# Optimization experiments

Measured on AMD Instinct MI355X. Metric: run time of the kernel, lower is better.

## Reference

```python
import jax, jax.numpy as jnp
import numpy as np

T, H, I, E, TOPK = 1024, 1024, 2816, 16, 4


def setup_inputs() -> dict:
    key = jax.random.key(0)
    ks = jax.random.split(key, 5)
    s_h = 1.0 / np.sqrt(H)
    s_i = 1.0 / np.sqrt(I)
    return {
        "x": jax.random.normal(ks[0], (T, H), jnp.float32),
        "Wg": jax.random.normal(ks[1], (E, H), jnp.float32) * s_h,
        "gate_w": jax.random.normal(ks[2], (E, H, I), jnp.float32) * s_h,
        "up_w": jax.random.normal(ks[3], (E, H, I), jnp.float32) * s_h,
        "down_w": jax.random.normal(ks[4], (E, I, H), jnp.float32) * s_i,
        "top_k": TOPK,
    }


def reference(x, Wg, gate_w, up_w, down_w, top_k):
    # Router: softmax over expert logits, top-k, renormalize
    logits = x @ Wg.T                                   # [T, E]
    probs = jax.nn.softmax(logits, axis=-1)
    topk_w, topk_ids = jax.lax.top_k(probs, top_k)      # [T, K]
    topk_w = topk_w / jnp.sum(topk_w, axis=-1, keepdims=True)

    # Dense combine weights [T, E]: zero for unselected experts -> exact same
    # math as the per-token dispatch loop in the original module.
    n_tok = x.shape[0]
    combine = jnp.zeros((n_tok, Wg.shape[0]), x.dtype)
    combine = combine.at[jnp.arange(n_tok)[:, None], topk_ids].add(topk_w)

    # SwiGLU per expert, batched over the expert axis
    g = jax.nn.silu(jnp.einsum('th,ehi->eti', x, gate_w))  # [E, T, I]
    u = jnp.einsum('th,ehi->eti', x, up_w)                 # [E, T, I]
    y = jnp.einsum('eti,eih->eth', g * u, down_w)          # [E, T, H]

    # Weighted combine across experts
    return jnp.einsum('eth,te->th', y, combine)            # [T, H]
```

## Files before the change

kernel.cpp:

```cpp
#include <hip/hip_runtime.h>

static constexpr int cT = 1024;
static constexpr int cH = 1024;
static constexpr int cI = 2816;
static constexpr int cE = 16;
static constexpr int cK = 4;

typedef __attribute__((ext_vector_type(8))) short bf16x8;
typedef __attribute__((ext_vector_type(4))) float f32x4;
typedef __attribute__((ext_vector_type(4))) unsigned uint4v;
typedef __attribute__((ext_vector_type(2))) unsigned uint2v;

__device__ __forceinline__ unsigned f2bf(float f) {
  unsigned u = __float_as_uint(f);
  return (u + 0x7FFFu + ((u >> 16) & 1u)) >> 16;
}
__device__ __forceinline__ unsigned pack2(float lo, float hi) {
  return f2bf(lo) | (f2bf(hi) << 16);
}

__global__ __launch_bounds__(256) void xcast_kernel(
    const float* __restrict__ x, unsigned short* __restrict__ xb) {
  const int i = blockIdx.x * 256 + threadIdx.x;
  const float4* xv = (const float4*)x;
  const float4 a = xv[i * 2], b = xv[i * 2 + 1];
  uint4v o;
  o.x = pack2(a.x, a.y); o.y = pack2(a.z, a.w);
  o.z = pack2(b.x, b.y); o.w = pack2(b.z, b.w);
  ((uint4v*)xb)[i] = o;
}

__global__ __launch_bounds__(64) void router_kernel(
    const float* __restrict__ x, const float* __restrict__ Wg,
    int* __restrict__ topk_id, float* __restrict__ topk_w,
    int* __restrict__ counts) {
  const int t = blockIdx.x;
  const int l = threadIdx.x;

  float xa[16];
#pragma unroll
  for (int i = 0; i < 16; ++i) xa[i] = x[(size_t)t * cH + l + 64 * i];

  float lg[16];
#pragma unroll
  for (int e = 0; e < 16; ++e) {
    float s = 0.f;
#pragma unroll
    for (int i = 0; i < 16; ++i) s += xa[i] * Wg[(size_t)e * cH + l + 64 * i];
#pragma unroll
    for (int d = 1; d < 64; d <<= 1) s += __shfl_xor(s, d);
    lg[e] = s;
  }

  if (l == 0) {
    int ids[4]; float vals[4];
    unsigned taken = 0;
#pragma unroll
    for (int j = 0; j < 4; ++j) {
      float m = -1e30f; int mi = 0;
#pragma unroll
      for (int e = 0; e < 16; ++e) {
        bool better = !((taken >> e) & 1u) && lg[e] > m;
        if (better) { m = lg[e]; mi = e; }
      }
      taken |= 1u << mi; ids[j] = mi; vals[j] = m;
    }
    const float mx = vals[0];
    float s = 0.f;
#pragma unroll
    for (int j = 0; j < 4; ++j) { vals[j] = __expf(vals[j] - mx); s += vals[j]; }
    const float inv = 1.f / s;
#pragma unroll
    for (int j = 0; j < 4; ++j) {
      topk_id[t * 4 + j] = ids[j];
      topk_w[t * 4 + j] = vals[j] * inv;
      atomicAdd(&counts[ids[j]], 1);
    }
  }
}

__global__ void scan_kernel(const int* __restrict__ counts,
                            int* __restrict__ offsets) {
  if (threadIdx.x == 0 && blockIdx.x == 0) {
    int acc = 0;
    for (int e = 0; e < cE; ++e) { offsets[e] = acc; acc += counts[e]; }
    offsets[cE] = acc;
  }
}

__global__ __launch_bounds__(256) void scatter_kernel(
    const int* __restrict__ topk_id, const float* __restrict__ topk_w,
    const int* __restrict__ offsets, int* __restrict__ cursor,
    int* __restrict__ pair_token, float* __restrict__ pair_w) {
  const int i = blockIdx.x * 256 + threadIdx.x;
  const int t = i >> 2;
  const int e = topk_id[i];
  const int pos = offsets[e] + atomicAdd(&cursor[e], 1);
  pair_token[pos] = t;
  pair_w[pos] = topk_w[i];
}

__global__ __launch_bounds__(256, 2) void gateup_kernel(
    const unsigned short* __restrict__ xb, const float* __restrict__ gw,
    const float* __restrict__ uw, const int* __restrict__ offsets,
    const int* __restrict__ pair_token, unsigned short* __restrict__ act) {
  const int e = blockIdx.y;
  const int off = offsets[e];
  const int n_e = offsets[e + 1] - off;
  if (n_e <= 0) return;
  const int nb = blockIdx.x * 64;
  const int tid = threadIdx.x;
  const int l = tid & 63, w = tid >> 6;
  const int wm = w * 64;

  __shared__ unsigned sB[2 * 2048];
  __shared__ int tokl[256];

  const int mat = tid >> 7;
  const int bg_ = (tid >> 4) & 7;
  const int bq  = tid & 15;
  const float* wp = (mat ? uw : gw) + (size_t)e * cH * cI + nb;

  for (int m0 = 0; m0 < n_e; m0 += 256) {
    const int rows = min(256, n_e - m0);
    tokl[tid] = pair_token[off + m0 + min(tid, rows - 1)];
    __syncthreads();

    const unsigned short* ap[4];
#pragma unroll
    for (int mi = 0; mi < 4; ++mi) {
      const int r = min(wm + mi * 16 + (l & 15), rows - 1);
      ap[mi] = xb + (size_t)tokl[r] * cH + (l >> 4) * 8;
    }

    f32x4 ag[4][4], au[4][4];
#pragma unroll
    for (int mi = 0; mi < 4; ++mi)
#pragma unroll
      for (int ni = 0; ni < 4; ++ni) {
        ag[mi][ni].x = 0.f; ag[mi][ni].y = 0.f; ag[mi][ni].z = 0.f; ag[mi][ni].w = 0.f;
        au[mi][ni].x = 0.f; au[mi][ni].y = 0.f; au[mi][ni].z = 0.f; au[mi][ni].w = 0.f;
      }

    for (int kt = 0; kt < cH / 64; ++kt) {
      bf16x8 av[4][2];
#pragma unroll
      for (int mi = 0; mi < 4; ++mi)
#pragma unroll
        for (int ks = 0; ks < 2; ++ks)
          av[mi][ks] = *(const bf16x8*)(ap[mi] + kt * 64 + ks * 32);

#pragma unroll
      for (int j = 0; j < 4; ++j) {
        const int c = bq + 16 * j;
        const float* p = wp + (size_t)(kt * 64 + bg_ * 8) * cI + c;
        const float f0 = p[0];
        const float f1 = p[(size_t)cI];
        const float f2 = p[(size_t)2 * cI];
        const float f3 = p[(size_t)3 * cI];
        const float f4 = p[(size_t)4 * cI];
        const float f5 = p[(size_t)5 * cI];
        const float f6 = p[(size_t)6 * cI];
        const float f7 = p[(size_t)7 * cI];
        uint4v P;
        P.x = pack2(f0, f1); P.y = pack2(f2, f3);
        P.z = pack2(f4, f5); P.w = pack2(f6, f7);
        *(uint4v*)&sB[mat * 2048 + (bg_ * 64 + c) * 4] = P;
      }
      __syncthreads();

#pragma unroll
      for (int ks = 0; ks < 2; ++ks) {
        const int gidx = ks * 4 + (l >> 4);
#pragma unroll
        for (int ni = 0; ni < 4; ++ni) {
          const int bi = (gidx * 64 + ni * 16 + (l & 15)) * 4;
          const bf16x8 bgf = *(const bf16x8*)&sB[bi];
          const bf16x8 buf_ = *(const bf16x8*)&sB[2048 + bi];
#pragma unroll
          for (int mi = 0; mi < 4; ++mi) {
            ag[mi][ni] = __builtin_amdgcn_mfma_f32_16x16x32_bf16(av[mi][ks], bgf, ag[mi][ni], 0, 0, 0);
            au[mi][ni] = __builtin_amdgcn_mfma_f32_16x16x32_bf16(av[mi][ks], buf_, au[mi][ni], 0, 0, 0);
          }
        }
      }
      __syncthreads();
    }

#pragma unroll
    for (int mi = 0; mi < 4; ++mi)
#pragma unroll
      for (int j = 0; j < 4; ++j) {
        const int er = m0 + wm + mi * 16 + (l >> 4) * 4 + j;
        if (er < n_e) {
#pragma unroll
          for (int ni = 0; ni < 4; ++ni) {
            const float g = ag[mi][ni][j], u = au[mi][ni][j];
            const float v = (g / (1.f + __expf(-g))) * u;
            act[(size_t)(off + er) * cI + nb + ni * 16 + (l & 15)] =
                (unsigned short)f2bf(v);
          }
        }
      }
  }
}

__global__ __launch_bounds__(256, 2) void down_kernel(
    const unsigned short* __restrict__ act, const float* __restrict__ dw,
    const int* __restrict__ offsets, const int* __restrict__ pair_token,
    const float* __restrict__ pair_w, float* __restrict__ out) {
  const int e = blockIdx.y;
  const int off = offsets[e];
  const int n_e = offsets[e + 1] - off;
  if (n_e <= 0) return;
  const int nb = blockIdx.x * 64;
  const int tid = threadIdx.x;
  const int l = tid & 63, w = tid >> 6;
  const int wm = w * 80;

  __shared__ unsigned sB[2048];

  const int bg_ = tid >> 5;
  const int bq  = (tid >> 1) & 15;
  const int bh  = tid & 1;
  const float* wp = dw + (size_t)e * cI * cH + nb;

  for (int m0 = 0; m0 < n_e; m0 += 320) {
    const unsigned short* ap[5];
#pragma unroll
    for (int mi = 0; mi < 5; ++mi) {
      const int r = min(m0 + wm + mi * 16 + (l & 15), n_e - 1);
      ap[mi] = act + (size_t)(off + r) * cI + (l >> 4) * 8;
    }

    f32x4 acc[5][4];
#pragma unroll
    for (int mi = 0; mi < 5; ++mi)
#pragma unroll
      for (int ni = 0; ni < 4; ++ni) {
        acc[mi][ni].x = 0.f; acc[mi][ni].y = 0.f;
        acc[mi][ni].z = 0.f; acc[mi][ni].w = 0.f;
      }

    for (int kt = 0; kt < cI / 64; ++kt) {
      bf16x8 av[5][2];
#pragma unroll
      for (int mi = 0; mi < 5; ++mi)
#pragma unroll
        for (int ks = 0; ks < 2; ++ks)
          av[mi][ks] = *(const bf16x8*)(ap[mi] + kt * 64 + ks * 32);

#pragma unroll
      for (int j = 0; j < 4; ++j) {
        const int c = bq + 16 * j;
        const float* p = wp + (size_t)(kt * 64 + bg_ * 8 + bh * 4) * cH + c;
        const float f0 = p[0];
        const float f1 = p[(size_t)cH];
        const float f2 = p[(size_t)2 * cH];
        const float f3 = p[(size_t)3 * cH];
        uint2v P;
        P.x = pack2(f0, f1); P.y = pack2(f2, f3);
        *(uint2v*)((char*)sB + (bg_ * 64 + c) * 16 + bh * 8) = P;
      }
      __syncthreads();

#pragma unroll
      for (int ks = 0; ks < 2; ++ks) {
        const int gidx = ks * 4 + (l >> 4);
#pragma unroll
        for (int ni = 0; ni < 4; ++ni) {
          const bf16x8 b = *(const bf16x8*)&sB[(gidx * 64 + ni * 16 + (l & 15)) * 4];
#pragma unroll
          for (int mi = 0; mi < 5; ++mi)
            acc[mi][ni] = __builtin_amdgcn_mfma_f32_16x16x32_bf16(av[mi][ks], b, acc[mi][ni], 0, 0, 0);
        }
      }
      __syncthreads();
    }

#pragma unroll
    for (int mi = 0; mi < 5; ++mi)
#pragma unroll
      for (int j = 0; j < 4; ++j) {
        const int er = m0 + wm + mi * 16 + (l >> 4) * 4 + j;
        if (er < n_e) {
          const int pr = off + er;
          const int t = pair_token[pr];
          const float wgt = pair_w[pr];
#pragma unroll
          for (int ni = 0; ni < 4; ++ni)
            atomicAdd(out + (size_t)t * cH + nb + ni * 16 + (l & 15),
                      wgt * acc[mi][ni][j]);
        }
      }
  }
}

extern "C" void kernel_launch(void* const* d_in, const int* in_sizes, int n_in,
                              void* d_out, int out_size, void* d_ws,
                              size_t ws_size, hipStream_t stream) {
  (void)in_sizes; (void)n_in; (void)out_size; (void)ws_size;
  const float* x = (const float*)d_in[0];
  const float* Wg = (const float*)d_in[1];
  const float* gw = (const float*)d_in[2];
  const float* uw = (const float*)d_in[3];
  const float* dw = (const float*)d_in[4];
  float* out = (float*)d_out;

  char* ws = (char*)d_ws;
  int* counts     = (int*)(ws + 0);
  int* cursor     = (int*)(ws + 64);
  int* offsets    = (int*)(ws + 128);
  int* topk_id    = (int*)(ws + 256);
  float* topk_w   = (float*)(ws + 256 + 16384);
  int* pair_token = (int*)(ws + 256 + 32768);
  float* pair_w   = (float*)(ws + 256 + 49152);
  unsigned short* act = (unsigned short*)(ws + 65792);
  unsigned short* xb  = (unsigned short*)(ws + 65792 + (size_t)4096 * 2816 * 2);

  hipMemsetAsync(ws, 0, 128, stream);
  hipMemsetAsync(d_out, 0, (size_t)cT * cH * sizeof(float), stream);

  xcast_kernel<<<cT * cH / (256 * 8), 256, 0, stream>>>(x, xb);
  router_kernel<<<cT, 64, 0, stream>>>(x, Wg, topk_id, topk_w, counts);
  scan_kernel<<<1, 1, 0, stream>>>(counts, offsets);
  scatter_kernel<<<cT * cK / 256, 256, 0, stream>>>(topk_id, topk_w, offsets,
                                                    cursor, pair_token, pair_w);
  gateup_kernel<<<dim3(cI / 64, cE), 256, 0, stream>>>(xb, gw, uw, offsets,
                                                       pair_token, act);
  down_kernel<<<dim3(cH / 64, cE), 256, 0, stream>>>(act, dw, offsets,
                                                     pair_token, pair_w, out);
}
```

Baseline: 454.2 us.

## Split MoE GEMMs over token chunks, prefetch weights, replace atomics with combine

Gate/up and down kernels now split each expert's tokens into 128-row chunks spread across three blocks per column strip, which raises parallelism and occupancy. Weight tiles are loaded with float4 reads, prefetched into registers one k-step ahead and written to a padded, double-buffered LDS layout, so one barrier per k-step replaces two. The down kernel writes unweighted per-pair outputs to a workspace, and a new combine kernel sums the four expert rows per token. This removes the atomic adds and the memset of the output, at the cost of an extra fp32 buffer and one more kernel launch. Each expert's weights are now streamed by several blocks instead of one, which adds redundant weight traffic.

```diff
diff --git a/kernel.cpp b/kernel.cpp
--- a/kernel.cpp
+++ b/kernel.cpp
@@ -8,8 +8,8 @@
 
 typedef __attribute__((ext_vector_type(8))) short bf16x8;
 typedef __attribute__((ext_vector_type(4))) float f32x4;
+typedef __attribute__((ext_vector_type(2))) unsigned uint2v;
 typedef __attribute__((ext_vector_type(4))) unsigned uint4v;
-typedef __attribute__((ext_vector_type(2))) unsigned uint2v;
 
 __device__ __forceinline__ unsigned f2bf(float f) {
   unsigned u = __float_as_uint(f);
@@ -17,6 +17,13 @@
 }
 __device__ __forceinline__ unsigned pack2(float lo, float hi) {
   return f2bf(lo) | (f2bf(hi) << 16);
+}
+
+__device__ __forceinline__ bf16x8 ld_bfrag(const unsigned* p) {
+  union { uint2v d[2]; bf16x8 v; } r;
+  r.d[0] = *(const uint2v*)p;
+  r.d[1] = *(const uint2v*)(p + 2);
+  return r.v;
 }
 
 __global__ __launch_bounds__(256) void xcast_kernel(
@@ -89,109 +96,113 @@
 }
 
 __global__ __launch_bounds__(256) void scatter_kernel(
-    const int* __restrict__ topk_id, const float* __restrict__ topk_w,
-    const int* __restrict__ offsets, int* __restrict__ cursor,
-    int* __restrict__ pair_token, float* __restrict__ pair_w) {
+    const int* __restrict__ topk_id, const int* __restrict__ offsets,
+    int* __restrict__ cursor, int* __restrict__ pair_token,
+    int* __restrict__ pair_pos) {
   const int i = blockIdx.x * 256 + threadIdx.x;
   const int t = i >> 2;
   const int e = topk_id[i];
   const int pos = offsets[e] + atomicAdd(&cursor[e], 1);
   pair_token[pos] = t;
-  pair_w[pos] = topk_w[i];
-}
-
-__global__ __launch_bounds__(256, 2) void gateup_kernel(
+  pair_pos[i] = pos;
+}
+
+__global__ __launch_bounds__(256, 3) void gateup_kernel(
     const unsigned short* __restrict__ xb, const float* __restrict__ gw,
     const float* __restrict__ uw, const int* __restrict__ offsets,
     const int* __restrict__ pair_token, unsigned short* __restrict__ act) {
   const int e = blockIdx.y;
   const int off = offsets[e];
   const int n_e = offsets[e + 1] - off;
-  if (n_e <= 0) return;
-  const int nb = blockIdx.x * 64;
-  const int tid = threadIdx.x;
-  const int l = tid & 63, w = tid >> 6;
-  const int wm = w * 64;
-
-  __shared__ unsigned sB[2 * 2048];
-  __shared__ int tokl[256];
-
-  const int mat = tid >> 7;
-  const int bg_ = (tid >> 4) & 7;
-  const int bq  = tid & 15;
-  const float* wp = (mat ? uw : gw) + (size_t)e * cH * cI + nb;
-
-  for (int m0 = 0; m0 < n_e; m0 += 256) {
-    const int rows = min(256, n_e - m0);
-    tokl[tid] = pair_token[off + m0 + min(tid, rows - 1)];
+  const int strip = blockIdx.x / 3;
+  const int c0 = (blockIdx.x % 3) * 128;
+  if (c0 >= n_e) return;
+  const int nb = strip * 64;
+  const int tid = threadIdx.x, l = tid & 63, w = tid >> 6;
+
+  __shared__ unsigned sB[2][2][2176];
+  __shared__ int tokl[128];
+
+  const int sa = tid >> 4;
+  const int sc = tid & 15;
+  const float* gb = gw + (size_t)e * cH * cI + nb + sc * 4;
+  const float* ub = uw + (size_t)e * cH * cI + nb + sc * 4;
+
+  for (int m0 = c0; m0 < n_e; m0 += 384) {
+    if (tid < 128) tokl[tid] = pair_token[off + min(m0 + tid, n_e - 1)];
     __syncthreads();
-
-    const unsigned short* ap[4];
-#pragma unroll
-    for (int mi = 0; mi < 4; ++mi) {
-      const int r = min(wm + mi * 16 + (l & 15), rows - 1);
-      ap[mi] = xb + (size_t)tokl[r] * cH + (l >> 4) * 8;
-    }
-
-    f32x4 ag[4][4], au[4][4];
-#pragma unroll
-    for (int mi = 0; mi < 4; ++mi)
+    const int rows = min(128, n_e - m0);
+
+    const unsigned short* ap[2];
+#pragma unroll
+    for (int mi = 0; mi < 2; ++mi) {
+      const int idx = min(w * 32 + mi * 16 + (l & 15), rows - 1);
+      ap[mi] = xb + (size_t)tokl[idx] * cH + (l >> 4) * 8;
+    }
+
+    f32x4 ag[2][4], au[2][4];
+#pragma unroll
+    for (int mi = 0; mi < 2; ++mi)
 #pragma unroll
       for (int ni = 0; ni < 4; ++ni) {
-        ag[mi][ni].x = 0.f; ag[mi][ni].y = 0.f; ag[mi][ni].z = 0.f; ag[mi][ni].w = 0.f;
-        au[mi][ni].x = 0.f; au[mi][ni].y = 0.f; au[mi][ni].z = 0.f; au[mi][ni].w = 0.f;
-      }
-
-    for (int kt = 0; kt < cH / 64; ++kt) {
-      bf16x8 av[4][2];
-#pragma unroll
-      for (int mi = 0; mi < 4; ++mi)
+        ag[mi][ni] = (f32x4){0.f, 0.f, 0.f, 0.f};
+        au[mi][ni] = (f32x4){0.f, 0.f, 0.f, 0.f};
+      }
+
+    float4 rg[4], ru[4];
+#pragma unroll
+    for (int j = 0; j < 4; ++j) {
+      rg[j] = *(const float4*)(gb + (size_t)(sa * 4 + j) * cI);
+      ru[j] = *(const float4*)(ub + (size_t)(sa * 4 + j) * cI);
+    }
+
+    for (int kt = 0; kt < 16; ++kt) {
+      const int cur = kt & 1;
+      const int wbase = (sc * 4) * 34 + sa * 2;
+#pragma unroll
+      for (int i = 0; i < 4; ++i) {
+        uint2v pg, pu;
+        pg.x = pack2(rg[0][i], rg[1][i]); pg.y = pack2(rg[2][i], rg[3][i]);
+        pu.x = pack2(ru[0][i], ru[1][i]); pu.y = pack2(ru[2][i], ru[3][i]);
+        *(uint2v*)&sB[cur][0][wbase + i * 34] = pg;
+        *(uint2v*)&sB[cur][1][wbase + i * 34] = pu;
+      }
+      if (kt + 1 < 16) {
+#pragma unroll
+        for (int j = 0; j < 4; ++j) {
+          rg[j] = *(const float4*)(gb + (size_t)((kt + 1) * 64 + sa * 4 + j) * cI);
+          ru[j] = *(const float4*)(ub + (size_t)((kt + 1) * 64 + sa * 4 + j) * cI);
+        }
+      }
+      __syncthreads();
+
+      bf16x8 av[2][2];
+#pragma unroll
+      for (int mi = 0; mi < 2; ++mi)
 #pragma unroll
         for (int ks = 0; ks < 2; ++ks)
           av[mi][ks] = *(const bf16x8*)(ap[mi] + kt * 64 + ks * 32);
 
 #pragma unroll
+      for (int ks = 0; ks < 2; ++ks)
+#pragma unroll
+        for (int ni = 0; ni < 4; ++ni) {
+          const int base = ((l & 15) + 16 * ni) * 34 + (l >> 4) * 4 + 16 * ks;
+          const bf16x8 bg = ld_bfrag(&sB[cur][0][base]);
+          const bf16x8 bu = ld_bfrag(&sB[cur][1][base]);
+#pragma unroll
+          for (int mi = 0; mi < 2; ++mi) {
+            ag[mi][ni] = __builtin_amdgcn_mfma_f32_16x16x32_bf16(av[mi][ks], bg, ag[mi][ni], 0, 0, 0);
+            au[mi][ni] = __builtin_amdgcn_mfma_f32_16x16x32_bf16(av[mi][ks], bu, au[mi][ni], 0, 0, 0);
+          }
+        }
+    }
+
+#pragma unroll
+    for (int mi = 0; mi < 2; ++mi)
+#pragma unroll
       for (int j = 0; j < 4; ++j) {
-        const int c = bq + 16 * j;
-        const float* p = wp + (size_t)(kt * 64 + bg_ * 8) * cI + c;
-        const float f0 = p[0];
-        const float f1 = p[(size_t)cI];
-        const float f2 = p[(size_t)2 * cI];
-        const float f3 = p[(size_t)3 * cI];
-        const float f4 = p[(size_t)4 * cI];
-        const float f5 = p[(size_t)5 * cI];
-        const float f6 = p[(size_t)6 * cI];
-        const float f7 = p[(size_t)7 * cI];
-        uint4v P;
-        P.x = pack2(f0, f1); P.y = pack2(f2, f3);
-        P.z = pack2(f4, f5); P.w = pack2(f6, f7);
-        *(uint4v*)&sB[mat * 2048 + (bg_ * 64 + c) * 4] = P;
-      }
-      __syncthreads();
-
-#pragma unroll
-      for (int ks = 0; ks < 2; ++ks) {
-        const int gidx = ks * 4 + (l >> 4);
-#pragma unroll
-        for (int ni = 0; ni < 4; ++ni) {
-          const int bi = (gidx * 64 + ni * 16 + (l & 15)) * 4;
-          const bf16x8 bgf = *(const bf16x8*)&sB[bi];
-          const bf16x8 buf_ = *(const bf16x8*)&sB[2048 + bi];
-#pragma unroll
-          for (int mi = 0; mi < 4; ++mi) {
-            ag[mi][ni] = __builtin_amdgcn_mfma_f32_16x16x32_bf16(av[mi][ks], bgf, ag[mi][ni], 0, 0, 0);
-            au[mi][ni] = __builtin_amdgcn_mfma_f32_16x16x32_bf16(av[mi][ks], buf_, au[mi][ni], 0, 0, 0);
-          }
-        }
-      }
-      __syncthreads();
-    }
-
-#pragma unroll
-    for (int mi = 0; mi < 4; ++mi)
-#pragma unroll
-      for (int j = 0; j < 4; ++j) {
-        const int er = m0 + wm + mi * 16 + (l >> 4) * 4 + j;
+        const int er = m0 + w * 32 + mi * 16 + (l >> 4) * 4 + j;
         if (er < n_e) {
 #pragma unroll
           for (int ni = 0; ni < 4; ++ni) {
@@ -205,95 +216,106 @@
   }
 }
 
-__global__ __launch_bounds__(256, 2) void down_kernel(
+__global__ __launch_bounds__(256, 4) void down_kernel(
     const unsigned short* __restrict__ act, const float* __restrict__ dw,
-    const int* __restrict__ offsets, const int* __restrict__ pair_token,
-    const float* __restrict__ pair_w, float* __restrict__ out) {
+    const int* __restrict__ offsets, float* __restrict__ yp) {
   const int e = blockIdx.y;
   const int off = offsets[e];
   const int n_e = offsets[e + 1] - off;
-  if (n_e <= 0) return;
-  const int nb = blockIdx.x * 64;
-  const int tid = threadIdx.x;
-  const int l = tid & 63, w = tid >> 6;
-  const int wm = w * 80;
-
-  __shared__ unsigned sB[2048];
-
-  const int bg_ = tid >> 5;
-  const int bq  = (tid >> 1) & 15;
-  const int bh  = tid & 1;
-  const float* wp = dw + (size_t)e * cI * cH + nb;
-
-  for (int m0 = 0; m0 < n_e; m0 += 320) {
-    const unsigned short* ap[5];
-#pragma unroll
-    for (int mi = 0; mi < 5; ++mi) {
-      const int r = min(m0 + wm + mi * 16 + (l & 15), n_e - 1);
+  const int strip = blockIdx.x / 3;
+  const int c0 = (blockIdx.x % 3) * 128;
+  if (c0 >= n_e) return;
+  const int nb = strip * 64;
+  const int tid = threadIdx.x, l = tid & 63, w = tid >> 6;
+
+  __shared__ unsigned sB[2][2176];
+
+  const int sa = tid >> 4, sc = tid & 15;
+  const float* db = dw + (size_t)e * cI * cH + nb + sc * 4;
+
+  for (int m0 = c0; m0 < n_e; m0 += 384) {
+    const int rows = min(128, n_e - m0);
+    const unsigned short* ap[2];
+#pragma unroll
+    for (int mi = 0; mi < 2; ++mi) {
+      const int r = min(m0 + w * 32 + mi * 16 + (l & 15), m0 + rows - 1);
       ap[mi] = act + (size_t)(off + r) * cI + (l >> 4) * 8;
     }
 
-    f32x4 acc[5][4];
-#pragma unroll
-    for (int mi = 0; mi < 5; ++mi)
-#pragma unroll
-      for (int ni = 0; ni < 4; ++ni) {
-        acc[mi][ni].x = 0.f; acc[mi][ni].y = 0.f;
-        acc[mi][ni].z = 0.f; acc[mi][ni].w = 0.f;
-      }
+    f32x4 acc[2][4];
+#pragma unroll
+    for (int mi = 0; mi < 2; ++mi)
+#pragma unroll
+      for (int ni = 0; ni < 4; ++ni) acc[mi][ni] = (f32x4){0.f, 0.f, 0.f, 0.f};
+
+    float4 rd[4];
+#pragma unroll
+    for (int j = 0; j < 4; ++j)
+      rd[j] = *(const float4*)(db + (size_t)(sa * 4 + j) * cH);
 
     for (int kt = 0; kt < cI / 64; ++kt) {
-      bf16x8 av[5][2];
-#pragma unroll
-      for (int mi = 0; mi < 5; ++mi)
+      const int cur = kt & 1;
+      const int wbase = (sc * 4) * 34 + sa * 2;
+#pragma unroll
+      for (int i = 0; i < 4; ++i) {
+        uint2v p;
+        p.x = pack2(rd[0][i], rd[1][i]); p.y = pack2(rd[2][i], rd[3][i]);
+        *(uint2v*)&sB[cur][wbase + i * 34] = p;
+      }
+      if (kt + 1 < cI / 64) {
+#pragma unroll
+        for (int j = 0; j < 4; ++j)
+          rd[j] = *(const float4*)(db + (size_t)((kt + 1) * 64 + sa * 4 + j) * cH);
+      }
+      __syncthreads();
+
+      bf16x8 av[2][2];
+#pragma unroll
+      for (int mi = 0; mi < 2; ++mi)
 #pragma unroll
         for (int ks = 0; ks < 2; ++ks)
           av[mi][ks] = *(const bf16x8*)(ap[mi] + kt * 64 + ks * 32);
 
 #pragma unroll
+      for (int ks = 0; ks < 2; ++ks)
+#pragma unroll
+        for (int ni = 0; ni < 4; ++ni) {
+          const int base = ((l & 15) + 16 * ni) * 34 + (l >> 4) * 4 + 16 * ks;
+          const bf16x8 b = ld_bfrag(&sB[cur][base]);
+#pragma unroll
+          for (int mi = 0; mi < 2; ++mi)
+            acc[mi][ni] = __builtin_amdgcn_mfma_f32_16x16x32_bf16(av[mi][ks], b, acc[mi][ni], 0, 0, 0);
+        }
+    }
+
+#pragma unroll
+    for (int mi = 0; mi < 2; ++mi)
+#pragma unroll
       for (int j = 0; j < 4; ++j) {
-        const int c = bq + 16 * j;
-        const float* p = wp + (size_t)(kt * 64 + bg_ * 8 + bh * 4) * cH + c;
-        const float f0 = p[0];
-        const float f1 = p[(size_t)cH];
-        const float f2 = p[(size_t)2 * cH];
-        const float f3 = p[(size_t)3 * cH];
-        uint2v P;
-        P.x = pack2(f0, f1); P.y = pack2(f2, f3);
-        *(uint2v*)((char*)sB + (bg_ * 64 + c) * 16 + bh * 8) = P;
-      }
-      __syncthreads();
-
-#pragma unroll
-      for (int ks = 0; ks < 2; ++ks) {
-        const int gidx = ks * 4 + (l >> 4);
-#pragma unroll
-        for (int ni = 0; ni < 4; ++ni) {
-          const bf16x8 b = *(const bf16x8*)&sB[(gidx * 64 + ni * 16 + (l & 15)) * 4];
-#pragma unroll
-          for (int mi = 0; mi < 5; ++mi)
-            acc[mi][ni] = __builtin_amdgcn_mfma_f32_16x16x32_bf16(av[mi][ks], b, acc[mi][ni], 0, 0, 0);
-        }
-      }
-      __syncthreads();
-    }
-
-#pragma unroll
-    for (int mi = 0; mi < 5; ++mi)
-#pragma unroll
-      for (int j = 0; j < 4; ++j) {
-        const int er = m0 + wm + mi * 16 + (l >> 4) * 4 + j;
+        const int er = m0 + w * 32 + mi * 16 + (l >> 4) * 4 + j;
         if (er < n_e) {
-          const int pr = off + er;
-          const int t = pair_token[pr];
-          const float wgt = pair_w[pr];
 #pragma unroll
           for (int ni = 0; ni < 4; ++ni)
-            atomicAdd(out + (size_t)t * cH + nb + ni * 16 + (l & 15),
-                      wgt * acc[mi][ni][j]);
-        }
-      }
-  }
+            yp[(size_t)(off + er) * cH + nb + ni * 16 + (l & 15)] = acc[mi][ni][j];
+        }
+      }
+  }
+}
+
+__global__ __launch_bounds__(256) void combine_kernel(
+    const float* __restrict__ yp, const int* __restrict__ pair_pos,
+    const float* __restrict__ topk_w, float* __restrict__ out) {
+  const int t = blockIdx.x;
+  const int cb = threadIdx.x * 4;
+  float4 s = make_float4(0.f, 0.f, 0.f, 0.f);
+#pragma unroll
+  for (int j = 0; j < 4; ++j) {
+    const int pos = pair_pos[t * 4 + j];
+    const float wj = topk_w[t * 4 + j];
+    const float4 v = *(const float4*)(yp + (size_t)pos * cH + cb);
+    s.x += wj * v.x; s.y += wj * v.y; s.z += wj * v.z; s.w += wj * v.w;
+  }
+  *(float4*)(out + (size_t)t * cH + cb) = s;
 }
 
 extern "C" void kernel_launch(void* const* d_in, const int* in_sizes, int n_in,
@@ -314,20 +336,20 @@
   int* topk_id    = (int*)(ws + 256);
   float* topk_w   = (float*)(ws + 256 + 16384);
   int* pair_token = (int*)(ws + 256 + 32768);
-  float* pair_w   = (float*)(ws + 256 + 49152);
+  int* pair_pos   = (int*)(ws + 256 + 49152);
   unsigned short* act = (unsigned short*)(ws + 65792);
   unsigned short* xb  = (unsigned short*)(ws + 65792 + (size_t)4096 * 2816 * 2);
+  float* yp = (float*)(ws + 65792 + (size_t)4096 * 2816 * 2 + (size_t)cT * cH * 2);
 
   hipMemsetAsync(ws, 0, 128, stream);
-  hipMemsetAsync(d_out, 0, (size_t)cT * cH * sizeof(float), stream);
 
   xcast_kernel<<<cT * cH / (256 * 8), 256, 0, stream>>>(x, xb);
   router_kernel<<<cT, 64, 0, stream>>>(x, Wg, topk_id, topk_w, counts);
   scan_kernel<<<1, 1, 0, stream>>>(counts, offsets);
-  scatter_kernel<<<cT * cK / 256, 256, 0, stream>>>(topk_id, topk_w, offsets,
-                                                    cursor, pair_token, pair_w);
-  gateup_kernel<<<dim3(cI / 64, cE), 256, 0, stream>>>(xb, gw, uw, offsets,
-                                                       pair_token, act);
-  down_kernel<<<dim3(cH / 64, cE), 256, 0, stream>>>(act, dw, offsets,
-                                                     pair_token, pair_w, out);
-}
+  scatter_kernel<<<cT * cK / 256, 256, 0, stream>>>(topk_id, offsets, cursor,
+                                                    pair_token, pair_pos);
+  gateup_kernel<<<dim3(44 * 3, cE), 256, 0, stream>>>(xb, gw, uw, offsets,
+                                                      pair_token, act);
+  down_kernel<<<dim3(16 * 3, cE), 256, 0, stream>>>(act, dw, offsets, yp);
+  combine_kernel<<<cT, 256, 0, stream>>>(yp, pair_pos, topk_w, out);
+}
```

Result: faster. 408.8 us (-10.0%).
